# Performance work log

Hardware: AMD Instinct MI355X
Metric: run time of the kernel (lower is better)

The kernel has to match this reference:

```python
import jax, jax.numpy as jnp
import numpy as np

N_NODES = 100000
D = 256
B = 64
EPG = 1024           # edges per query group in the last (pruned) layer
E1 = B * EPG         # 65536
E0 = 65536
K = 256              # max_edges


def setup_inputs() -> dict:
    key = jax.random.key(0)
    ks = jax.random.split(key, 20)
    # last-layer edges: sorted by eg_idx, exactly EPG edges per query group
    eg_idx1 = np.repeat(np.arange(B, dtype=np.int32), EPG)
    node_i1 = np.asarray(jax.random.randint(ks[0], (E1,), 0, N_NODES, dtype=jnp.int32))
    node_j1 = np.asarray(jax.random.randint(ks[1], (E1,), 0, N_NODES, dtype=jnp.int32))
    edges1 = np.zeros((E1, 8), dtype=np.int32)
    edges1[:, 0] = eg_idx1; edges1[:, 6] = node_i1; edges1[:, 7] = node_j1
    # earlier-layer edges (no pruning, any order)
    edges0 = np.zeros((E0, 8), dtype=np.int32)
    edges0[:, 0] = np.asarray(jax.random.randint(ks[2], (E0,), 0, B, dtype=jnp.int32))
    edges0[:, 6] = np.asarray(jax.random.randint(ks[3], (E0,), 0, N_NODES, dtype=jnp.int32))
    edges0[:, 7] = np.asarray(jax.random.randint(ks[4], (E0,), 0, N_NODES, dtype=jnp.int32))

    rn = lambda k, s, sc=1.0: (jax.random.normal(k, s, dtype=jnp.float32) * sc)
    return {
        "attended_nodes": jax.random.randint(ks[5], (B, 2), 0, N_NODES, dtype=jnp.int32),
        "node_score": jax.random.uniform(ks[6], (N_NODES,), dtype=jnp.float32),
        "edges0": jnp.asarray(edges0),
        "edges1": jnp.asarray(edges1),
        "rel_emb0": rn(ks[7], (E0, D)),
        "rel_emb1": rn(ks[8], (E1, D)),
        "memorized_embedding": rn(ks[9], (N_NODES, D)),
        "query_src_ts_emb": rn(ks[10], (B, D)),
        "query_rel_emb": rn(ks[11], (B, D)),
        "Wl": rn(ks[12], (4 * D, 2 * D), np.sqrt(2.0 / (4 * D))),
        "bl": rn(ks[13], (2 * D,), 0.01),
        "Wr": rn(ks[14], (4 * D, 2 * D), np.sqrt(2.0 / (4 * D))),
        "br": rn(ks[15], (2 * D,), 0.01),
        "Wc": rn(ks[16], (2 * D, 2 * D), np.sqrt(2.0 / (4 * D))),
        "bc": rn(ks[17], (2 * D,), 0.01),
        "Wlin": rn(ks[18], (D, D), np.sqrt(2.0 / D)),
        "blin": rn(ks[19], (D,), 0.01),
        "max_edges": K,
    }


def _g_score(hi, hj, rel, qs, qr, Wl, bl, Wr, br, Wc, bc):
    # bilinear MLP score: sum(LReLU(L @ Wl) * ((LReLU(R @ Wr)) @ Wc), -1)
    left = jnp.concatenate([hi, rel, qs, qr], axis=-1)   # [E, 4D]
    right = jnp.concatenate([hj, rel, qs, qr], axis=-1)  # [E, 4D]
    l = jax.nn.leaky_relu(left @ Wl + bl)                # [E, 2D]
    r = jax.nn.leaky_relu(right @ Wr + br) @ Wc + bc     # [E, 2D]
    return jnp.sum(l * r, axis=-1)                       # [E]


def _att_score(edges, emb, rel, qs_tab, qr_tab, Wl, bl, Wr, br, Wc, bc):
    hi = emb[edges[:, 6]]
    hj = emb[edges[:, 7]]
    qs = qs_tab[edges[:, 0]]
    qr = qr_tab[edges[:, 0]]
    return _g_score(hi, hj, rel, qs, qr, Wl, bl, Wr, br, Wc, bc)


def _segment_softmax(logits, seg, num_seg):
    m = jax.ops.segment_max(logits, seg, num_segments=num_seg)
    e = jnp.exp(logits - m[seg])
    s = jax.ops.segment_sum(e, seg, num_segments=num_seg)
    return e / s[seg]


def _update_nodes(edges, emb, logits):
    # aggregate source embeddings into targets, weighted by attention;
    # nodes with no incoming edge keep their old embedding.
    n = emb.shape[0]
    agg = jax.ops.segment_sum(logits[:, None] * emb[edges[:, 6]], edges[:, 7], num_segments=n)
    cnt = jax.ops.segment_sum(jnp.ones_like(logits), edges[:, 7], num_segments=n)
    return jnp.where((cnt > 0)[:, None], agg, emb)


def reference(attended_nodes, node_score, edges0, edges1, rel_emb0, rel_emb1,
              memorized_embedding, query_src_ts_emb, query_rel_emb,
              Wl, bl, Wr, br, Wc, bc, Wlin, blin, max_edges):
    n_nodes = memorized_embedding.shape[0]
    # ---- last layer: attention + segmented softmax over source node ----
    logits1 = _att_score(edges1, memorized_embedding, rel_emb1,
                         query_src_ts_emb, query_rel_emb, Wl, bl, Wr, br, Wc, bc)
    sm1 = _segment_softmax(logits1, edges1[:, 6], n_nodes)
    src_att = node_score[edges1[:, 6]]
    target_att = sm1 * src_att
    # ---- per-query top-k pruning (groups are contiguous, equal size EPG) ----
    b = B
    vals = target_att.reshape(b, EPG)
    pruned_att2, idx = jax.lax.top_k(vals, max_edges)              # [B, K]
    orig_indices = (jnp.arange(b, dtype=idx.dtype)[:, None] * EPG + idx).reshape(-1)
    pruned_att = pruned_att2.reshape(-1)                           # [B*K]
    pruned_edges = edges1[orig_indices]
    sm_pruned = sm1[orig_indices]
    # ---- node score aggregation ('sum') ----
    updated_node_score = jax.ops.segment_sum(sm_pruned * pruned_att,
                                             pruned_edges[:, 7], num_segments=n_nodes)
    # ---- propagate representations along pruned edges ----
    emb = _update_nodes(pruned_edges, memorized_embedding, sm_pruned)
    # ---- earlier layers (reversed) ----
    logits0 = _att_score(edges0, emb, rel_emb0, query_src_ts_emb, query_rel_emb,
                         Wl, bl, Wr, br, Wc, bc)
    sm0 = _segment_softmax(logits0, edges0[:, 6], n_nodes)
    emb = _update_nodes(edges0, emb, sm0)
    # ---- bypass: linear + LeakyReLU between steps ----
    emb = jax.nn.leaky_relu(emb @ Wlin + blin)
    return updated_node_score, emb, pruned_edges, orig_indices
```

## Files before the change

### kernel.cpp

```cpp
#include <hip/hip_runtime.h>
#include <math.h>


#define NNODES 100000
#define DDIM   256
#define NH     512
#define NGROUP 64
#define EPG    1024
#define E1N    65536
#define E0N    65536
#define KTOP   256

typedef __attribute__((ext_vector_type(8))) _Float16 h8v;
typedef __attribute__((ext_vector_type(4))) float f32x4;

__device__ __forceinline__ float lrelu(float x) { return x > 0.0f ? x : 0.01f * x; }

__device__ __forceinline__ unsigned fenc(float f) {
  unsigned u = __float_as_uint(f);
  return (u & 0x80000000u) ? ~u : (u | 0x80000000u);
}
__device__ __forceinline__ float fdec(unsigned k) {
  unsigned u = (k & 0x80000000u) ? (k & 0x7FFFFFFFu) : ~k;
  return __uint_as_float(u);
}

__device__ __forceinline__ void splitf(float v, unsigned short& h, unsigned short& l) {
  _Float16 hh = (_Float16)v;
  _Float16 ll = (_Float16)(v - (float)hh);
  h = __builtin_bit_cast(unsigned short, hh);
  l = __builtin_bit_cast(unsigned short, ll);
}

__device__ __forceinline__ f32x4 mfma16(h8v a, h8v b, f32x4 c) {
  return __builtin_amdgcn_mfma_f32_16x16x32_f16(a, b, c, 0, 0, 0);
}

__device__ __forceinline__ void pack8(uint4 a, uint4 b, uint4& ph, uint4& pl) {
  float v[8] = {__uint_as_float(a.x), __uint_as_float(a.y),
                __uint_as_float(a.z), __uint_as_float(a.w),
                __uint_as_float(b.x), __uint_as_float(b.y),
                __uint_as_float(b.z), __uint_as_float(b.w)};
  unsigned short h[8], l[8];
#pragma unroll
  for (int d = 0; d < 8; ++d) splitf(v[d], h[d], l[d]);
  ph = make_uint4((unsigned)h[0] | ((unsigned)h[1] << 16),
                  (unsigned)h[2] | ((unsigned)h[3] << 16),
                  (unsigned)h[4] | ((unsigned)h[5] << 16),
                  (unsigned)h[6] | ((unsigned)h[7] << 16));
  pl = make_uint4((unsigned)l[0] | ((unsigned)l[1] << 16),
                  (unsigned)l[2] | ((unsigned)l[3] << 16),
                  (unsigned)l[4] | ((unsigned)l[5] << 16),
                  (unsigned)l[6] | ((unsigned)l[7] << 16));
}

__global__ __launch_bounds__(512)
void qterm_kernel(const float* __restrict__ qse, const float* __restrict__ qre,
                  const float* __restrict__ Wl, const float* __restrict__ bl,
                  const float* __restrict__ Wr, const float* __restrict__ br,
                  float* __restrict__ qtl, float* __restrict__ qtr)
{
  const int g = blockIdx.x;
  const int o = threadIdx.x;
  __shared__ float sq[DDIM];
  __shared__ float sr[DDIM];
  if (o < DDIM) sq[o] = qse[(size_t)g * DDIM + o];
  else          sr[o - DDIM] = qre[(size_t)g * DDIM + (o - DDIM)];
  __syncthreads();
  float al = bl[o], ar = br[o];
  for (int k = 0; k < DDIM; ++k) {
    float a = sq[k], b = sr[k];
    al += a * Wl[(size_t)(512 + k) * NH + o] + b * Wl[(size_t)(768 + k) * NH + o];
    ar += a * Wr[(size_t)(512 + k) * NH + o] + b * Wr[(size_t)(768 + k) * NH + o];
  }
  qtl[(size_t)g * NH + o] = al;
  qtr[(size_t)g * NH + o] = ar;
}

__global__ __launch_bounds__(256)
void wprep_kernel(const float* __restrict__ Wl, const float* __restrict__ Wr,
                  const float* __restrict__ Wc,
                  unsigned short* __restrict__ WltH, unsigned short* __restrict__ WltL,
                  unsigned short* __restrict__ WrtH, unsigned short* __restrict__ WrtL,
                  unsigned short* __restrict__ WctH, unsigned short* __restrict__ WctL)
{
  __shared__ float shv[32][33];
  const int mtx = blockIdx.y;
  const int ti = blockIdx.x >> 4;
  const int tj = blockIdx.x & 15;
  const float* W = mtx == 0 ? Wl : (mtx == 1 ? Wr : Wc);
  unsigned short* OH = mtx == 0 ? WltH : (mtx == 1 ? WrtH : WctH);
  unsigned short* OL = mtx == 0 ? WltL : (mtx == 1 ? WrtL : WctL);
  const int t = threadIdx.x;
  const int r = t >> 3, c4 = (t & 7) * 4;
  *(float4*)&shv[r][c4] = *(const float4*)(W + (size_t)(ti * 32 + r) * 512 + tj * 32 + c4);
  __syncthreads();
  unsigned short h[4], l[4];
#pragma unroll
  for (int q = 0; q < 4; ++q) splitf(shv[c4 + q][r], h[q], l[q]);
  const size_t off = (size_t)(tj * 32 + r) * 512 + ti * 32 + c4;
  *(uint2*)(OH + off) = make_uint2((unsigned)h[0] | ((unsigned)h[1] << 16),
                                   (unsigned)h[2] | ((unsigned)h[3] << 16));
  *(uint2*)(OL + off) = make_uint2((unsigned)l[0] | ((unsigned)l[1] << 16),
                                   (unsigned)l[2] | ((unsigned)l[3] << 16));
}

__global__ __launch_bounds__(256)
void wlinprep_kernel(const float* __restrict__ Wlin, unsigned short* __restrict__ WlinT)
{
  __shared__ float shv[32][33];
  const int ti = blockIdx.x >> 3;
  const int tj = blockIdx.x & 7;
  const int t = threadIdx.x;
  const int r = t >> 3, c4 = (t & 7) * 4;
  *(float4*)&shv[r][c4] = *(const float4*)(Wlin + (size_t)(ti * 32 + r) * 256 + tj * 32 + c4);
  __syncthreads();
  unsigned short o[4];
#pragma unroll
  for (int q = 0; q < 4; ++q)
    o[q] = __builtin_bit_cast(unsigned short, (_Float16)shv[c4 + q][r]);
  *(uint2*)(WlinT + (size_t)(tj * 32 + r) * 256 + ti * 32 + c4) =
      make_uint2((unsigned)o[0] | ((unsigned)o[1] << 16),
                 (unsigned)o[2] | ((unsigned)o[3] << 16));
}

template<int SPLIT>
__global__ __launch_bounds__(512, 2)
void fused_score_kernel(const int* __restrict__ edges,
                        const float* __restrict__ embA,
                        const float* __restrict__ embB,
                        const int* __restrict__ cntSel,
                        const float* __restrict__ rel,
                        const unsigned short* __restrict__ BrH,
                        const unsigned short* __restrict__ BrL,
                        const unsigned short* __restrict__ BcH,
                        const unsigned short* __restrict__ BcL,
                        const unsigned short* __restrict__ BlH,
                        const unsigned short* __restrict__ BlL,
                        const float* __restrict__ qtr,
                        const float* __restrict__ qtl,
                        const float* __restrict__ bcv,
                        float* __restrict__ logits,
                        unsigned* __restrict__ mkey)
{
  constexpr int NG = 4096;
  __shared__ uint4 planesv[(SPLIT ? 2 : 1) * NG];
  __shared__ float red[8][64];
  __shared__ int sidxJ[64], sidxI[64], sgrp[64];

  const int tid  = threadIdx.x;
  const int lane = tid & 63;
  const int w    = tid >> 6;
  const int arow = lane & 15;
  const int grp  = lane >> 4;
  const int col0 = w * 64;
  const int rb   = blockIdx.x * 64;

  const int srow = tid >> 3;
  const int gs   = tid & 7;
  const int ssw  = srow & 7;

  if (tid < 64) {
    const int* er = edges + (size_t)(rb + tid) * 8;
    sgrp[tid]  = er[0];
    sidxI[tid] = er[6];
    sidxJ[tid] = er[7];
  }
  __syncthreads();

  const float* baseR = rel + (size_t)(rb + srow) * DDIM - 256;

  auto rowbase = [&](int idx) -> const float* {
    const float* b = (cntSel && cntSel[idx] > 0) ? embA : embB;
    return b + (size_t)idx * DDIM;
  };

  uint4 ai[16];
  {
    const float* bI = rowbase(sidxI[srow]);
#pragma unroll
    for (int q = 0; q < 8; ++q) {
      const int lg = (q * 8 + gs) ^ ssw;
      const int kf = lg << 3;
      const float* s = (lg < 32) ? (bI + kf) : (baseR + kf);
      ai[2 * q]     = ((const uint4*)s)[0];
      ai[2 * q + 1] = ((const uint4*)s)[1];
    }
  }

  {
    const float* bJ = rowbase(sidxJ[srow]);
#pragma unroll
    for (int q = 0; q < 8; ++q) {
      const int g  = q * 8 + gs;
      const int lg = g ^ ssw;
      const int kf = lg << 3;
      const float* s = (lg < 32) ? (bJ + kf) : (baseR + kf);
      uint4 f0 = ((const uint4*)s)[0];
      uint4 f1 = ((const uint4*)s)[1];
      uint4 ph, pl;
      pack8(f0, f1, ph, pl);
      planesv[srow * 64 + g] = ph;
      if (SPLIT) planesv[NG + srow * 64 + g] = pl;
    }
  }
  __syncthreads();

  const unsigned short* hiP = (const unsigned short*)planesv;
  const unsigned short* loP = hiP + (size_t)NG * 8;

  auto gemm = [&](const unsigned short* BH, const unsigned short* BL,
                  f32x4 (&acc)[4][4]) {
    for (int ks = 0; ks < 16; ++ks) {
      const int k0 = ks * 32 + grp * 8;
      h8v bh[4], bl[4];
#pragma unroll
      for (int nt = 0; nt < 4; ++nt) {
        const size_t boff = (size_t)(col0 + nt * 16 + arow) * 512 + k0;
        bh[nt] = *(const h8v*)(BH + boff);
        if (SPLIT) bl[nt] = *(const h8v*)(BL + boff);
      }
#pragma unroll
      for (int mt = 0; mt < 4; ++mt) {
        const int row = mt * 16 + arow;
        const int gh = (ks * 4 + grp) ^ (row & 7);
        h8v h = *(const h8v*)(hiP + row * 512 + gh * 8);
        h8v l;
        if (SPLIT) l = *(const h8v*)(loP + row * 512 + gh * 8);
#pragma unroll
        for (int nt = 0; nt < 4; ++nt) {
          acc[mt][nt] = mfma16(h, bh[nt], acc[mt][nt]);
          if (SPLIT) {
            acc[mt][nt] = mfma16(h, bl[nt], acc[mt][nt]);
            acc[mt][nt] = mfma16(l, bh[nt], acc[mt][nt]);
          }
        }
      }
    }
  };

  f32x4 a1[4][4];
#pragma unroll
  for (int a = 0; a < 4; ++a)
#pragma unroll
    for (int b = 0; b < 4; ++b) a1[a][b] = (f32x4)0.0f;
  gemm(BrH, BrL, a1);
  __syncthreads();

  {
    unsigned short* hiW = (unsigned short*)planesv;
    unsigned short* loW = hiW + (size_t)NG * 8;
#pragma unroll
    for (int mt = 0; mt < 4; ++mt)
#pragma unroll
      for (int nt = 0; nt < 4; ++nt) {
        const int c = col0 + nt * 16 + arow;
#pragma unroll
        for (int reg = 0; reg < 4; ++reg) {
          const int row = mt * 16 + grp * 4 + reg;
          float v = lrelu(a1[mt][nt][reg] + qtr[(size_t)sgrp[row] * NH + c]);
          unsigned short h, l;
          splitf(v, h, l);
          const int off = row * 512 + (((c >> 3) ^ (row & 7)) << 3) + (c & 7);
          hiW[off] = h;
          if (SPLIT) loW[off] = l;
        }
      }
  }
  __syncthreads();

  f32x4 ro[4][4];
#pragma unroll
  for (int a = 0; a < 4; ++a)
#pragma unroll
    for (int b = 0; b < 4; ++b) ro[a][b] = (f32x4)0.0f;
  gemm(BcH, BcL, ro);
#pragma unroll
  for (int nt = 0; nt < 4; ++nt) {
    const float bcval = bcv[col0 + nt * 16 + arow];
#pragma unroll
    for (int mt = 0; mt < 4; ++mt)
#pragma unroll
      for (int reg = 0; reg < 4; ++reg) ro[mt][nt][reg] += bcval;
  }
  __syncthreads();

#pragma unroll
  for (int q = 0; q < 8; ++q) {
    uint4 ph, pl;
    pack8(ai[2 * q], ai[2 * q + 1], ph, pl);
    planesv[srow * 64 + q * 8 + gs] = ph;
    if (SPLIT) planesv[NG + srow * 64 + q * 8 + gs] = pl;
  }
  __syncthreads();

  f32x4 a3[4][4];
#pragma unroll
  for (int a = 0; a < 4; ++a)
#pragma unroll
    for (int b = 0; b < 4; ++b) a3[a][b] = (f32x4)0.0f;
  gemm(BlH, BlL, a3);
#pragma unroll
  for (int mt = 0; mt < 4; ++mt) {
#pragma unroll
    for (int reg = 0; reg < 4; ++reg) {
      const int row = mt * 16 + grp * 4 + reg;
      const int g = sgrp[row];
      float s = 0.0f;
#pragma unroll
      for (int nt = 0; nt < 4; ++nt) {
        const int c = col0 + nt * 16 + arow;
        float v = lrelu(a3[mt][nt][reg] + qtl[(size_t)g * NH + c]);
        s += v * ro[mt][nt][reg];
      }
      s += __shfl_xor(s, 1); s += __shfl_xor(s, 2);
      s += __shfl_xor(s, 4); s += __shfl_xor(s, 8);
      if ((lane & 15) == 0) red[w][row] = s;
    }
  }
  __syncthreads();
  if (tid < 64) {
    float s = 0.0f;
#pragma unroll
    for (int p = 0; p < 8; ++p) s += red[p][tid];
    logits[rb + tid] = s;
    atomicMax(mkey + sidxI[tid], fenc(s));
  }
}

__global__ void smax_exp_kernel(const int* __restrict__ edges, const float* __restrict__ logits,
                                const unsigned* __restrict__ mkey, float* __restrict__ ssum,
                                float* __restrict__ sm, int* __restrict__ cnt, int E)
{
  int e = blockIdx.x * blockDim.x + threadIdx.x;
  if (e < E) {
    int s = edges[(size_t)e * 8 + 6];
    float ev = expf(logits[e] - fdec(mkey[s]));
    sm[e] = ev;
    atomicAdd(ssum + s, ev);
    if (cnt) atomicAdd(cnt + edges[(size_t)e * 8 + 7], 1);
  }
}

__global__ void smax_norm_kernel(const int* __restrict__ edges, const float* __restrict__ ssum,
                                 float* __restrict__ sm, const float* __restrict__ nscore,
                                 float* __restrict__ ta, int E)
{
  int e = blockIdx.x * blockDim.x + threadIdx.x;
  if (e < E) {
    int s = edges[(size_t)e * 8 + 6];
    float v = sm[e] / ssum[s];
    sm[e] = v;
    if (ta) ta[e] = v * nscore[s];
  }
}

__global__ __launch_bounds__(256)
void topk_kernel(const float* __restrict__ ta, const float* __restrict__ sm1,
                 const int* __restrict__ edges1,
                 float* __restrict__ out0, float* __restrict__ out2,
                 float* __restrict__ out3, float* __restrict__ smp,
                 int* __restrict__ prn_i, int* __restrict__ prn_j,
                 int* __restrict__ cnt1)
{
  __shared__ float v[EPG];
  __shared__ int   ix[EPG];
  const int g = blockIdx.x, tid = threadIdx.x;
  for (int t = tid; t < EPG; t += 256) { v[t] = ta[(size_t)g * EPG + t]; ix[t] = t; }
  __syncthreads();
  for (int k = 2; k <= EPG; k <<= 1) {
    for (int j = k >> 1; j > 0; j >>= 1) {
      for (int t = tid; t < EPG; t += 256) {
        int l = t ^ j;
        if (l > t) {
          float va = v[t], vb = v[l];
          int ia = ix[t], ib = ix[l];
          bool aFirst = (va > vb) || (va == vb && ia < ib);
          bool up = ((t & k) == 0);
          bool sw = up ? !aFirst : aFirst;
          if (sw) { v[t] = vb; ix[t] = ib; v[l] = va; ix[l] = ia; }
        }
      }
      __syncthreads();
    }
  }
  const int r = tid;
  const int oi = ix[r];
  const float val = v[r];
  const int orig = g * EPG + oi;
  out3[(size_t)g * KTOP + r] = (float)orig;
  const int* er = edges1 + (size_t)orig * 8;
#pragma unroll
  for (int c = 0; c < 8; ++c)
    out2[((size_t)(g * KTOP + r)) * 8 + c] = (float)er[c];
  const int ii = er[6], jj = er[7];
  const float smv = sm1[orig];
  smp[(size_t)g * KTOP + r] = smv;
  prn_i[(size_t)g * KTOP + r] = ii;
  prn_j[(size_t)g * KTOP + r] = jj;
  atomicAdd(out0 + jj, smv * val);
  atomicAdd(cnt1 + jj, 1);
}

__global__ void scatter_kernel(const int* __restrict__ idx_i,
                               const int* __restrict__ idx_j,
                               const float* __restrict__ w,
                               const float* __restrict__ semb,
                               float* __restrict__ agg)
{
  const int e0 = blockIdx.x * 4;
  const int o = threadIdx.x;
#pragma unroll
  for (int q = 0; q < 4; ++q) {
    const int e = e0 + q;
    const int i = idx_i[e];
    const int j = idx_j[e];
    atomicAdd(agg + (size_t)j * DDIM + o, w[e] * semb[(size_t)i * DDIM + o]);
  }
}

__global__ void scatter0_kernel(const int* __restrict__ edges,
                                const float* __restrict__ sm,
                                const float* __restrict__ ssum,
                                const float* __restrict__ agg1,
                                const float* __restrict__ mememb,
                                const int* __restrict__ cnt1,
                                float* __restrict__ out)
{
  const int e0 = blockIdx.x * 4;
  const int o = threadIdx.x;
#pragma unroll
  for (int q = 0; q < 4; ++q) {
    const int e = e0 + q;
    const int i = edges[(size_t)e * 8 + 6];
    const int j = edges[(size_t)e * 8 + 7];
    const float wv = sm[e] / ssum[i];
    const float* src = ((cnt1[i] > 0) ? agg1 : mememb) + (size_t)i * DDIM;
    atomicAdd(out + (size_t)j * DDIM + o, wv * src[o]);
  }
}

__global__ __launch_bounds__(512)
void final_mfma_kernel(const float* __restrict__ agg1, const float* __restrict__ mememb,
                       const int* __restrict__ cnt1,
                       const float* __restrict__ agg0, const int* __restrict__ cnt0,
                       const unsigned short* __restrict__ WlinT,
                       const float* __restrict__ blin, float* __restrict__ out)
{
  __shared__ int ssel[128];
  const int tid  = threadIdx.x;
  const int lane = tid & 63;
  const int wid  = tid >> 6;
  const int wm = wid >> 2, wn = wid & 3;
  const int rb = blockIdx.x * 128;
  const int arow = lane & 15;
  const int kgrp = (lane >> 4) * 8;
  const int row0 = wm * 64;
  const int col0 = wn * 64;

  if (tid < 128) {
    int r = rb + tid;
    int rc = (r < NNODES) ? r : 0;
    int s = 0;
    if (cnt0[rc] > 0) s = 2;
    else if (cnt1[rc] > 0) s = 1;
    ssel[tid] = s;
  }
  __syncthreads();

  f32x4 acc[4][4];
#pragma unroll
  for (int a = 0; a < 4; ++a)
#pragma unroll
    for (int b = 0; b < 4; ++b) acc[a][b] = (f32x4)0.0f;

  for (int ks = 0; ks < 8; ++ks) {
    const int k0 = ks * 32 + kgrp;
    h8v ah[4], bh[4];
#pragma unroll
    for (int nt = 0; nt < 4; ++nt)
      bh[nt] = *(const h8v*)(WlinT + (size_t)(col0 + nt * 16 + arow) * 256 + k0);
#pragma unroll
    for (int mt = 0; mt < 4; ++mt) {
      const int rl = row0 + mt * 16 + arow;
      int r = rb + rl;
      int rc = (r < NNODES) ? r : (NNODES - 1);
      const int sel = ssel[rl];
      const float* base = (sel == 2) ? agg0 : ((sel == 1) ? agg1 : mememb);
      const float* src = base + (size_t)rc * DDIM + k0;
      float4 f0 = *(const float4*)src;
      float4 f1 = *(const float4*)(src + 4);
      float v[8] = {f0.x, f0.y, f0.z, f0.w, f1.x, f1.y, f1.z, f1.w};
      h8v h;
#pragma unroll
      for (int d = 0; d < 8; ++d) h[d] = (_Float16)v[d];
      ah[mt] = h;
    }
#pragma unroll
    for (int mt = 0; mt < 4; ++mt)
#pragma unroll
      for (int nt = 0; nt < 4; ++nt)
        acc[mt][nt] = mfma16(ah[mt], bh[nt], acc[mt][nt]);
  }

  float bl4[4];
#pragma unroll
  for (int nt = 0; nt < 4; ++nt) bl4[nt] = blin[col0 + nt * 16 + arow];

#pragma unroll
  for (int mt = 0; mt < 4; ++mt)
#pragma unroll
    for (int reg = 0; reg < 4; ++reg) {
      const int r = rb + row0 + mt * 16 + (lane >> 4) * 4 + reg;
      if (r < NNODES) {
#pragma unroll
        for (int nt = 0; nt < 4; ++nt) {
          const int c = col0 + nt * 16 + arow;
          out[(size_t)r * DDIM + c] = lrelu(acc[mt][nt][reg] + bl4[nt]);
        }
      }
    }
}

extern "C" void kernel_launch(void* const* d_in, const int* in_sizes, int n_in,
                              void* d_out, int out_size, void* d_ws, size_t ws_size,
                              hipStream_t stream)
{
  (void)in_sizes; (void)n_in; (void)out_size; (void)ws_size;

  const float* node_score = (const float*)d_in[1];
  const int*   edges0 = (const int*)d_in[2];
  const int*   edges1 = (const int*)d_in[3];
  const float* rel0   = (const float*)d_in[4];
  const float* rel1   = (const float*)d_in[5];
  const float* mememb = (const float*)d_in[6];
  const float* qse    = (const float*)d_in[7];
  const float* qre    = (const float*)d_in[8];
  const float* Wl     = (const float*)d_in[9];
  const float* bl     = (const float*)d_in[10];
  const float* Wr     = (const float*)d_in[11];
  const float* br     = (const float*)d_in[12];
  const float* Wc     = (const float*)d_in[13];
  const float* bc     = (const float*)d_in[14];
  const float* Wlin   = (const float*)d_in[15];
  const float* blin   = (const float*)d_in[16];

  float* out0 = (float*)d_out;
  float* out1 = out0 + NNODES;
  float* out2 = out1 + (size_t)NNODES * DDIM;
  float* out3 = out2 + (size_t)NGROUP * KTOP * 8;

  char* wptr = (char*)d_ws;
  auto alloc = [&](size_t bytes) -> char* {
    char* p = wptr;
    wptr += (bytes + 255) & ~(size_t)255;
    return p;
  };
  float*    qtl     = (float*)alloc((size_t)NGROUP * NH * 4);
  float*    qtr     = (float*)alloc((size_t)NGROUP * NH * 4);
  float*    logits1 = (float*)alloc((size_t)E1N * 4);
  float*    sm1     = (float*)alloc((size_t)E1N * 4);
  float*    ta      = (float*)alloc((size_t)E1N * 4);
  float*    logits0 = (float*)alloc((size_t)E0N * 4);
  float*    sm0     = (float*)alloc((size_t)E0N * 4);
  unsigned* mkey    = (unsigned*)alloc((size_t)NNODES * 4);
  float*    ssum    = (float*)alloc((size_t)NNODES * 4);
  int*      cnt1    = (int*)alloc((size_t)NNODES * 4);
  int*      cnt0    = (int*)alloc((size_t)NNODES * 4);
  float*    smp     = (float*)alloc((size_t)NGROUP * KTOP * 4);
  int*      prn_i   = (int*)alloc((size_t)NGROUP * KTOP * 4);
  int*      prn_j   = (int*)alloc((size_t)NGROUP * KTOP * 4);
  float*    agg1    = (float*)alloc((size_t)NNODES * DDIM * 4);

  unsigned short* WltH = (unsigned short*)alloc((size_t)512 * 512 * 2);
  unsigned short* WltL = (unsigned short*)alloc((size_t)512 * 512 * 2);
  unsigned short* WrtH = (unsigned short*)alloc((size_t)512 * 512 * 2);
  unsigned short* WrtL = (unsigned short*)alloc((size_t)512 * 512 * 2);
  unsigned short* WctH = (unsigned short*)alloc((size_t)512 * 512 * 2);
  unsigned short* WctL = (unsigned short*)alloc((size_t)512 * 512 * 2);
  unsigned short* WlnT = (unsigned short*)alloc((size_t)256 * 256 * 2);

  (void)hipMemsetAsync(agg1, 0, (size_t)NNODES * DDIM * 4, stream);
  (void)hipMemsetAsync(cnt1, 0, (size_t)NNODES * 4, stream);
  (void)hipMemsetAsync(mkey, 0, (size_t)NNODES * 4, stream);
  (void)hipMemsetAsync(ssum, 0, (size_t)NNODES * 4, stream);
  (void)hipMemsetAsync(out0, 0, (size_t)NNODES * 4, stream);

  qterm_kernel<<<NGROUP, 512, 0, stream>>>(qse, qre, Wl, bl, Wr, br, qtl, qtr);
  {
    dim3 g(256, 3);
    wprep_kernel<<<g, 256, 0, stream>>>(Wl, Wr, Wc, WltH, WltL, WrtH, WrtL, WctH, WctL);
  }
  wlinprep_kernel<<<64, 256, 0, stream>>>(Wlin, WlnT);

  fused_score_kernel<1><<<E1N / 64, 512, 0, stream>>>(
      edges1, mememb, mememb, nullptr, rel1,
      WrtH, WrtL, WctH, WctL, WltH, WltL,
      qtr, qtl, bc, logits1, mkey);

  smax_exp_kernel<<<E1N / 256, 256, 0, stream>>>(edges1, logits1, mkey, ssum, sm1,
                                                 nullptr, E1N);
  smax_norm_kernel<<<E1N / 256, 256, 0, stream>>>(edges1, ssum, sm1, node_score, ta, E1N);
  topk_kernel<<<NGROUP, 256, 0, stream>>>(ta, sm1, edges1, out0, out2, out3,
                                          smp, prn_i, prn_j, cnt1);
  scatter_kernel<<<NGROUP * KTOP / 4, 256, 0, stream>>>(prn_i, prn_j, smp,
                                                        mememb, agg1);

  (void)hipMemsetAsync(mkey, 0, (size_t)NNODES * 4, stream);
  (void)hipMemsetAsync(ssum, 0, (size_t)NNODES * 4, stream);
  (void)hipMemsetAsync(cnt0, 0, (size_t)NNODES * 4, stream);
  (void)hipMemsetAsync(out1, 0, (size_t)NNODES * DDIM * 4, stream);

  fused_score_kernel<0><<<E0N / 64, 512, 0, stream>>>(
      edges0, agg1, mememb, cnt1, rel0,
      WrtH, WrtL, WctH, WctL, WltH, WltL,
      qtr, qtl, bc, logits0, mkey);

  smax_exp_kernel<<<E0N / 256, 256, 0, stream>>>(edges0, logits0, mkey, ssum, sm0,
                                                 cnt0, E0N);
  scatter0_kernel<<<E0N / 4, 256, 0, stream>>>(edges0, sm0, ssum, agg1, mememb,
                                               cnt1, out1);
  final_mfma_kernel<<<(NNODES + 127) / 128, 512, 0, stream>>>(agg1, mememb, cnt1,
                                                              out1, cnt0,
                                                              WlnT, blin, out1);
}
```

Before: 1.035 ms.

## Halve rows per block in fused score kernel to raise occupancy

The fused score kernel now handles 32 edges per block instead of 64. Its shared-memory planes, accumulator arrays and row tiles shrink to match, and launch bounds rise to 4 blocks per SM. The left-input rows are no longer kept in registers across the first two GEMMs; they are reloaded from global memory and staged into shared memory right before the third GEMM, which frees about 64 registers per thread. The aim is more resident waves to hide gather latency, at the cost of reloading every weight tile twice as often per edge and re-fetching the gathered rows.

```diff
diff --git a/kernel.cpp b/kernel.cpp
--- a/kernel.cpp
+++ b/kernel.cpp
@@ -125,7 +125,7 @@
 }
 
 template<int SPLIT>
-__global__ __launch_bounds__(512, 2)
+__global__ __launch_bounds__(512, 4)
 void fused_score_kernel(const int* __restrict__ edges,
                         const float* __restrict__ embA,
                         const float* __restrict__ embB,
@@ -143,10 +143,10 @@
                         float* __restrict__ logits,
                         unsigned* __restrict__ mkey)
 {
-  constexpr int NG = 4096;
+  constexpr int NG = 2048;
   __shared__ uint4 planesv[(SPLIT ? 2 : 1) * NG];
-  __shared__ float red[8][64];
-  __shared__ int sidxJ[64], sidxI[64], sgrp[64];
+  __shared__ float red[8][32];
+  __shared__ int sidxJ[32], sidxI[32], sgrp[32];
 
   const int tid  = threadIdx.x;
   const int lane = tid & 63;
@@ -154,13 +154,13 @@
   const int arow = lane & 15;
   const int grp  = lane >> 4;
   const int col0 = w * 64;
-  const int rb   = blockIdx.x * 64;
-
-  const int srow = tid >> 3;
-  const int gs   = tid & 7;
+  const int rb   = blockIdx.x * 32;
+
+  const int srow = tid >> 4;
+  const int gs   = tid & 15;
   const int ssw  = srow & 7;
 
-  if (tid < 64) {
+  if (tid < 32) {
     const int* er = edges + (size_t)(rb + tid) * 8;
     sgrp[tid]  = er[0];
     sidxI[tid] = er[6];
@@ -175,27 +175,14 @@
     return b + (size_t)idx * DDIM;
   };
 
-  uint4 ai[16];
-  {
-    const float* bI = rowbase(sidxI[srow]);
-#pragma unroll
-    for (int q = 0; q < 8; ++q) {
-      const int lg = (q * 8 + gs) ^ ssw;
-      const int kf = lg << 3;
-      const float* s = (lg < 32) ? (bI + kf) : (baseR + kf);
-      ai[2 * q]     = ((const uint4*)s)[0];
-      ai[2 * q + 1] = ((const uint4*)s)[1];
-    }
-  }
-
-  {
-    const float* bJ = rowbase(sidxJ[srow]);
-#pragma unroll
-    for (int q = 0; q < 8; ++q) {
-      const int g  = q * 8 + gs;
+  auto stage = [&](const int* idxArr) {
+    const float* bX = rowbase(idxArr[srow]);
+#pragma unroll
+    for (int q = 0; q < 4; ++q) {
+      const int g  = q * 16 + gs;
       const int lg = g ^ ssw;
       const int kf = lg << 3;
-      const float* s = (lg < 32) ? (bJ + kf) : (baseR + kf);
+      const float* s = (lg < 32) ? (bX + kf) : (baseR + kf);
       uint4 f0 = ((const uint4*)s)[0];
       uint4 f1 = ((const uint4*)s)[1];
       uint4 ph, pl;
@@ -203,45 +190,52 @@
       planesv[srow * 64 + g] = ph;
       if (SPLIT) planesv[NG + srow * 64 + g] = pl;
     }
-  }
+  };
+
+  stage(sidxJ);
   __syncthreads();
 
   const unsigned short* hiP = (const unsigned short*)planesv;
   const unsigned short* loP = hiP + (size_t)NG * 8;
 
   auto gemm = [&](const unsigned short* BH, const unsigned short* BL,
-                  f32x4 (&acc)[4][4]) {
+                  f32x4 (&acc)[2][4]) {
     for (int ks = 0; ks < 16; ++ks) {
       const int k0 = ks * 32 + grp * 8;
-      h8v bh[4], bl[4];
-#pragma unroll
-      for (int nt = 0; nt < 4; ++nt) {
-        const size_t boff = (size_t)(col0 + nt * 16 + arow) * 512 + k0;
-        bh[nt] = *(const h8v*)(BH + boff);
-        if (SPLIT) bl[nt] = *(const h8v*)(BL + boff);
-      }
-#pragma unroll
-      for (int mt = 0; mt < 4; ++mt) {
-        const int row = mt * 16 + arow;
-        const int gh = (ks * 4 + grp) ^ (row & 7);
-        h8v h = *(const h8v*)(hiP + row * 512 + gh * 8);
-        h8v l;
-        if (SPLIT) l = *(const h8v*)(loP + row * 512 + gh * 8);
-#pragma unroll
-        for (int nt = 0; nt < 4; ++nt) {
-          acc[mt][nt] = mfma16(h, bh[nt], acc[mt][nt]);
-          if (SPLIT) {
-            acc[mt][nt] = mfma16(h, bl[nt], acc[mt][nt]);
-            acc[mt][nt] = mfma16(l, bh[nt], acc[mt][nt]);
+#pragma unroll
+      for (int nh = 0; nh < 2; ++nh) {
+        h8v bh[2], bl[2];
+#pragma unroll
+        for (int p = 0; p < 2; ++p) {
+          const int nt = nh * 2 + p;
+          const size_t boff = (size_t)(col0 + nt * 16 + arow) * 512 + k0;
+          bh[p] = *(const h8v*)(BH + boff);
+          if (SPLIT) bl[p] = *(const h8v*)(BL + boff);
+        }
+#pragma unroll
+        for (int mt = 0; mt < 2; ++mt) {
+          const int row = mt * 16 + arow;
+          const int gh = (ks * 4 + grp) ^ (row & 7);
+          h8v h = *(const h8v*)(hiP + row * 512 + gh * 8);
+          h8v l;
+          if (SPLIT) l = *(const h8v*)(loP + row * 512 + gh * 8);
+#pragma unroll
+          for (int p = 0; p < 2; ++p) {
+            const int nt = nh * 2 + p;
+            acc[mt][nt] = mfma16(h, bh[p], acc[mt][nt]);
+            if (SPLIT) {
+              acc[mt][nt] = mfma16(h, bl[p], acc[mt][nt]);
+              acc[mt][nt] = mfma16(l, bh[p], acc[mt][nt]);
+            }
           }
         }
       }
     }
   };
 
-  f32x4 a1[4][4];
-#pragma unroll
-  for (int a = 0; a < 4; ++a)
+  f32x4 a1[2][4];
+#pragma unroll
+  for (int a = 0; a < 2; ++a)
 #pragma unroll
     for (int b = 0; b < 4; ++b) a1[a][b] = (f32x4)0.0f;
   gemm(BrH, BrL, a1);
@@ -251,7 +245,7 @@
     unsigned short* hiW = (unsigned short*)planesv;
     unsigned short* loW = hiW + (size_t)NG * 8;
 #pragma unroll
-    for (int mt = 0; mt < 4; ++mt)
+    for (int mt = 0; mt < 2; ++mt)
 #pragma unroll
       for (int nt = 0; nt < 4; ++nt) {
         const int c = col0 + nt * 16 + arow;
@@ -269,9 +263,9 @@
   }
   __syncthreads();
 
-  f32x4 ro[4][4];
-#pragma unroll
-  for (int a = 0; a < 4; ++a)
+  f32x4 ro[2][4];
+#pragma unroll
+  for (int a = 0; a < 2; ++a)
 #pragma unroll
     for (int b = 0; b < 4; ++b) ro[a][b] = (f32x4)0.0f;
   gemm(BcH, BcL, ro);
@@ -279,29 +273,23 @@
   for (int nt = 0; nt < 4; ++nt) {
     const float bcval = bcv[col0 + nt * 16 + arow];
 #pragma unroll
-    for (int mt = 0; mt < 4; ++mt)
+    for (int mt = 0; mt < 2; ++mt)
 #pragma unroll
       for (int reg = 0; reg < 4; ++reg) ro[mt][nt][reg] += bcval;
   }
   __syncthreads();
 
-#pragma unroll
-  for (int q = 0; q < 8; ++q) {
-    uint4 ph, pl;
-    pack8(ai[2 * q], ai[2 * q + 1], ph, pl);
-    planesv[srow * 64 + q * 8 + gs] = ph;
-    if (SPLIT) planesv[NG + srow * 64 + q * 8 + gs] = pl;
-  }
-  __syncthreads();
-
-  f32x4 a3[4][4];
-#pragma unroll
-  for (int a = 0; a < 4; ++a)
+  stage(sidxI);
+  __syncthreads();
+
+  f32x4 a3[2][4];
+#pragma unroll
+  for (int a = 0; a < 2; ++a)
 #pragma unroll
     for (int b = 0; b < 4; ++b) a3[a][b] = (f32x4)0.0f;
   gemm(BlH, BlL, a3);
 #pragma unroll
-  for (int mt = 0; mt < 4; ++mt) {
+  for (int mt = 0; mt < 2; ++mt) {
 #pragma unroll
     for (int reg = 0; reg < 4; ++reg) {
       const int row = mt * 16 + grp * 4 + reg;
@@ -319,7 +307,7 @@
     }
   }
   __syncthreads();
-  if (tid < 64) {
+  if (tid < 32) {
     float s = 0.0f;
 #pragma unroll
     for (int p = 0; p < 8; ++p) s += red[p][tid];
@@ -593,7 +581,7 @@
   }
   wlinprep_kernel<<<64, 256, 0, stream>>>(Wlin, WlnT);
 
-  fused_score_kernel<1><<<E1N / 64, 512, 0, stream>>>(
+  fused_score_kernel<1><<<E1N / 32, 512, 0, stream>>>(
       edges1, mememb, mememb, nullptr, rel1,
       WrtH, WrtL, WctH, WctL, WltH, WltL,
       qtr, qtl, bc, logits1, mkey);
@@ -611,7 +599,7 @@
   (void)hipMemsetAsync(cnt0, 0, (size_t)NNODES * 4, stream);
   (void)hipMemsetAsync(out1, 0, (size_t)NNODES * DDIM * 4, stream);
 
-  fused_score_kernel<0><<<E0N / 64, 512, 0, stream>>>(
+  fused_score_kernel<0><<<E0N / 32, 512, 0, stream>>>(
       edges0, agg1, mememb, cnt1, rel0,
       WrtH, WrtL, WctH, WctL, WltH, WltL,
       qtr, qtl, bc, logits0, mkey);
```

Result: slower. 1.513 ms (+46.2%).

## Zero only touched agg rows and fold softmax normalization into top-k

Applied to the files above, without the earlier changes.

The full-size memset of the 100000x256 aggregation buffer is replaced by a small kernel that zeroes only the rows named by the pruned edges' destination nodes. This relies on later kernels reading agg1 only for nodes with a nonzero count. The separate softmax-normalize pass is removed: the top-k kernel now computes sm/ssum*node_score on load and normalizes the selected sm values itself, which drops the ta buffer. A `#pragma unroll 2` is also added to the score GEMM k-loop.

```diff
diff --git a/kernel.cpp b/kernel.cpp
--- a/kernel.cpp
+++ b/kernel.cpp
@@ -211,6 +211,7 @@
 
   auto gemm = [&](const unsigned short* BH, const unsigned short* BL,
                   f32x4 (&acc)[4][4]) {
+#pragma unroll 2
     for (int ks = 0; ks < 16; ++ks) {
       const int k0 = ks * 32 + grp * 8;
       h8v bh[4], bl[4];
@@ -342,21 +343,9 @@
   }
 }
 
-__global__ void smax_norm_kernel(const int* __restrict__ edges, const float* __restrict__ ssum,
-                                 float* __restrict__ sm, const float* __restrict__ nscore,
-                                 float* __restrict__ ta, int E)
-{
-  int e = blockIdx.x * blockDim.x + threadIdx.x;
-  if (e < E) {
-    int s = edges[(size_t)e * 8 + 6];
-    float v = sm[e] / ssum[s];
-    sm[e] = v;
-    if (ta) ta[e] = v * nscore[s];
-  }
-}
-
 __global__ __launch_bounds__(256)
-void topk_kernel(const float* __restrict__ ta, const float* __restrict__ sm1,
+void topk_kernel(const float* __restrict__ sm1, const float* __restrict__ ssum,
+                 const float* __restrict__ nscore,
                  const int* __restrict__ edges1,
                  float* __restrict__ out0, float* __restrict__ out2,
                  float* __restrict__ out3, float* __restrict__ smp,
@@ -366,7 +355,12 @@
   __shared__ float v[EPG];
   __shared__ int   ix[EPG];
   const int g = blockIdx.x, tid = threadIdx.x;
-  for (int t = tid; t < EPG; t += 256) { v[t] = ta[(size_t)g * EPG + t]; ix[t] = t; }
+  for (int t = tid; t < EPG; t += 256) {
+    const int e = g * EPG + t;
+    const int s = edges1[(size_t)e * 8 + 6];
+    v[t] = (sm1[e] / ssum[s]) * nscore[s];
+    ix[t] = t;
+  }
   __syncthreads();
   for (int k = 2; k <= EPG; k <<= 1) {
     for (int j = k >> 1; j > 0; j >>= 1) {
@@ -394,12 +388,18 @@
   for (int c = 0; c < 8; ++c)
     out2[((size_t)(g * KTOP + r)) * 8 + c] = (float)er[c];
   const int ii = er[6], jj = er[7];
-  const float smv = sm1[orig];
+  const float smv = sm1[orig] / ssum[ii];
   smp[(size_t)g * KTOP + r] = smv;
   prn_i[(size_t)g * KTOP + r] = ii;
   prn_j[(size_t)g * KTOP + r] = jj;
   atomicAdd(out0 + jj, smv * val);
   atomicAdd(cnt1 + jj, 1);
+}
+
+__global__ void zero_rows_kernel(const int* __restrict__ prn_j, float* __restrict__ agg)
+{
+  const int j = prn_j[blockIdx.x];
+  agg[(size_t)j * DDIM + threadIdx.x] = 0.0f;
 }
 
 __global__ void scatter_kernel(const int* __restrict__ idx_i,
@@ -560,7 +560,6 @@
   float*    qtr     = (float*)alloc((size_t)NGROUP * NH * 4);
   float*    logits1 = (float*)alloc((size_t)E1N * 4);
   float*    sm1     = (float*)alloc((size_t)E1N * 4);
-  float*    ta      = (float*)alloc((size_t)E1N * 4);
   float*    logits0 = (float*)alloc((size_t)E0N * 4);
   float*    sm0     = (float*)alloc((size_t)E0N * 4);
   unsigned* mkey    = (unsigned*)alloc((size_t)NNODES * 4);
@@ -580,7 +579,6 @@
   unsigned short* WctL = (unsigned short*)alloc((size_t)512 * 512 * 2);
   unsigned short* WlnT = (unsigned short*)alloc((size_t)256 * 256 * 2);
 
-  (void)hipMemsetAsync(agg1, 0, (size_t)NNODES * DDIM * 4, stream);
   (void)hipMemsetAsync(cnt1, 0, (size_t)NNODES * 4, stream);
   (void)hipMemsetAsync(mkey, 0, (size_t)NNODES * 4, stream);
   (void)hipMemsetAsync(ssum, 0, (size_t)NNODES * 4, stream);
@@ -600,9 +598,10 @@
 
   smax_exp_kernel<<<E1N / 256, 256, 0, stream>>>(edges1, logits1, mkey, ssum, sm1,
                                                  nullptr, E1N);
-  smax_norm_kernel<<<E1N / 256, 256, 0, stream>>>(edges1, ssum, sm1, node_score, ta, E1N);
-  topk_kernel<<<NGROUP, 256, 0, stream>>>(ta, sm1, edges1, out0, out2, out3,
+  topk_kernel<<<NGROUP, 256, 0, stream>>>(sm1, ssum, node_score, edges1,
+                                          out0, out2, out3,
                                           smp, prn_i, prn_j, cnt1);
+  zero_rows_kernel<<<NGROUP * KTOP, 256, 0, stream>>>(prn_j, agg1);
   scatter_kernel<<<NGROUP * KTOP / 4, 256, 0, stream>>>(prn_i, prn_j, smp,
                                                         mememb, agg1);
 
```

Result: no change. 1.027 ms (-0.7%).
